# Optimization experiments

Measured on AMD Instinct MI355X. Metric: run time of the kernel, lower is better.

Reference implementation:

```python
import jax, jax.numpy as jnp
import numpy as np

B, N, C = 8, 900, 256
HEADS, P = 8, 4
BEV_H, BEV_W = 200, 200
RADIUS = 0.2


def setup_inputs() -> dict:
    key = jax.random.key(0)
    ks = jax.random.split(key, 6)
    return {
        'query': jax.random.normal(ks[0], (B, N, C), dtype=jnp.float32),
        'memory': jax.random.normal(ks[1], (B, BEV_H * BEV_W, C), dtype=jnp.float32),
        'reference_points': jax.random.uniform(ks[2], (B, N, 2), dtype=jnp.float32),
        'w_off': jax.random.normal(ks[3], (C, HEADS * P * 2), dtype=jnp.float32) * 0.02,
        'b_off': jnp.zeros((HEADS * P * 2,), jnp.float32),
        'w_wt': jax.random.normal(ks[4], (C, HEADS * P), dtype=jnp.float32) * 0.02,
        'b_wt': jnp.zeros((HEADS * P,), jnp.float32),
        'w_out': jax.random.normal(ks[5], (C, C), dtype=jnp.float32) * 0.02,
        'b_out': jnp.zeros((C,), jnp.float32),
        'bev_h': BEV_H,
        'bev_w': BEV_W,
    }


def reference(query, memory, reference_points, w_off, b_off, w_wt, b_wt, w_out, b_out, bev_h, bev_w):
    Bq, Nq, Cq = query.shape
    hd = Cq // HEADS
    # memory [B, H*W, C] -> per-head feature map flattened: [B, heads, HW, hd]
    feat = memory.transpose(0, 2, 1).reshape(Bq, HEADS, hd, bev_h * bev_w)
    feat = feat.transpose(0, 1, 3, 2)

    offsets = jnp.tanh(query @ w_off + b_off).reshape(Bq, Nq, HEADS, P, 2) * RADIUS
    weights = jax.nn.softmax((query @ w_wt + b_wt).reshape(Bq, Nq, HEADS, P), axis=-1)
    loc = reference_points[:, :, None, None, :2] + offsets  # [B,N,heads,P,2], normalized [0,1]

    # grid_sample(align_corners=False, zeros padding): pixel = p*size - 0.5
    x = loc[..., 0] * bev_w - 0.5
    y = loc[..., 1] * bev_h - 0.5
    x0f = jnp.floor(x)
    y0f = jnp.floor(y)
    x0 = x0f.astype(jnp.int32)
    y0 = y0f.astype(jnp.int32)
    fx = (x - x0f)[..., None]
    fy = (y - y0f)[..., None]

    def gather(xi, yi):
        valid = (xi >= 0) & (xi < bev_w) & (yi >= 0) & (yi < bev_h)
        idx = jnp.clip(yi, 0, bev_h - 1) * bev_w + jnp.clip(xi, 0, bev_w - 1)  # [B,N,heads,P]
        idx_t = idx.transpose(0, 2, 1, 3).reshape(Bq, HEADS, Nq * P)
        v = jnp.take_along_axis(feat, idx_t[..., None], axis=2)  # [B,heads,N*P,hd]
        v = v.reshape(Bq, HEADS, Nq, P, hd).transpose(0, 2, 1, 3, 4)  # [B,N,heads,P,hd]
        return v * valid.astype(v.dtype)[..., None]

    v00 = gather(x0, y0)
    v01 = gather(x0 + 1, y0)
    v10 = gather(x0, y0 + 1)
    v11 = gather(x0 + 1, y0 + 1)
    sampled = (v00 * (1 - fx) * (1 - fy) + v01 * fx * (1 - fy)
               + v10 * (1 - fx) * fy + v11 * fx * fy)  # [B,N,heads,P,hd]

    fused = (sampled * weights[..., None]).sum(axis=3).reshape(Bq, Nq, Cq)
    return fused @ w_out + b_out
```

## Files before the change

kernel.cpp:

```cpp
#include <hip/hip_runtime.h>
#include <math.h>

#define BB 8
#define NN 900
#define CC 256
#define HEADS 8
#define PP 4
#define BEV_H 200
#define BEV_W 200
#define HW (BEV_H * BEV_W)
#define HD 32
#define RADIUS 0.2f
#define M_TOT (BB * NN)

#define PROJ_AR 32
#define PROJ_BLOCKS (M_TOT / PROJ_AR)
#define PACK_BLOCKS 32
#define SR 16
#define SFS 280

typedef short s16x8 __attribute__((ext_vector_type(8)));
typedef float f32x4 __attribute__((ext_vector_type(4)));

static __device__ __forceinline__ unsigned short f2bf(float f) {
    unsigned int x = __float_as_uint(f);
    unsigned int r = x + 0x7FFFu + ((x >> 16) & 1u);
    return (unsigned short)(r >> 16);
}

__global__ __launch_bounds__(256) void proj_pack_kernel(
    const float* __restrict__ query,
    const float* __restrict__ refpts,
    const float* __restrict__ w_off,
    const float* __restrict__ b_off,
    const float* __restrict__ w_wt,
    const float* __restrict__ b_wt,
    const float* __restrict__ w_out,
    float* __restrict__ rec_w,
    int*   __restrict__ rec_i,
    unsigned short* __restrict__ Bp)
{
    const int t = threadIdx.x;

    if (blockIdx.x >= PROJ_BLOCKS) {
        const int g = (blockIdx.x - PROJ_BLOCKS) * 256 + t;
        const int n = g & 255, kg = g >> 8;
        unsigned int w[4];
        #pragma unroll
        for (int jj = 0; jj < 4; ++jj) {
            const unsigned int lo = f2bf(w_out[(size_t)(kg * 8 + jj * 2 + 0) * CC + n]);
            const unsigned int hi = f2bf(w_out[(size_t)(kg * 8 + jj * 2 + 1) * CC + n]);
            w[jj] = lo | (hi << 16);
        }
        uint4 v; v.x = w[0]; v.y = w[1]; v.z = w[2]; v.w = w[3];
        *(uint4*)&Bp[(size_t)g * 8] = v;
        return;
    }

    __shared__ float s_q[PROJ_AR][68];
    __shared__ float s_w[64][96];
    __shared__ float s_l[PROJ_AR][100];

    const int row0 = blockIdx.x * PROJ_AR;
    const int r  = t >> 3;
    const int cq = t & 7;

    float acc[12] = {};

    for (int k0 = 0; k0 < CC; k0 += 64) {
        __syncthreads();
        #pragma unroll
        for (int j = 0; j < 2; ++j) {
            const int e = (t + j * 256) * 4;
            const int rr = e >> 6, kk = e & 63;
            *(float4*)&s_q[rr][kk] =
                *(const float4*)&query[(size_t)(row0 + rr) * CC + k0 + kk];
        }
        #pragma unroll
        for (int j = 0; j < 4; ++j) {
            const int e = t + j * 256;
            const int kk = e >> 4, c4 = (e & 15) * 4;
            *(float4*)&s_w[kk][c4] =
                *(const float4*)&w_off[(size_t)(k0 + kk) * 64 + c4];
        }
        #pragma unroll
        for (int j = 0; j < 2; ++j) {
            const int e = t + j * 256;
            const int kk = e >> 3, c4 = (e & 7) * 4;
            *(float4*)&s_w[kk][64 + c4] =
                *(const float4*)&w_wt[(size_t)(k0 + kk) * 32 + c4];
        }
        __syncthreads();
        #pragma unroll 8
        for (int kk = 0; kk < 64; ++kk) {
            const float qv = s_q[r][kk];
            const float4 w0 = *(const float4*)&s_w[kk][cq * 12 + 0];
            const float4 w1 = *(const float4*)&s_w[kk][cq * 12 + 4];
            const float4 w2 = *(const float4*)&s_w[kk][cq * 12 + 8];
            acc[0]  += qv * w0.x; acc[1]  += qv * w0.y;
            acc[2]  += qv * w0.z; acc[3]  += qv * w0.w;
            acc[4]  += qv * w1.x; acc[5]  += qv * w1.y;
            acc[6]  += qv * w1.z; acc[7]  += qv * w1.w;
            acc[8]  += qv * w2.x; acc[9]  += qv * w2.y;
            acc[10] += qv * w2.z; acc[11] += qv * w2.w;
        }
    }

    #pragma unroll
    for (int j = 0; j < 12; ++j) {
        const int col = cq * 12 + j;
        const float bias = (col < 64) ? b_off[col] : b_wt[col - 64];
        s_l[r][col] = acc[j] + bias;
    }
    __syncthreads();

    {
        const int h = t & 7;
        const int bn = row0 + r;
        const float rx = refpts[(size_t)bn * 2 + 0];
        const float ry = refpts[(size_t)bn * 2 + 1];

        const float l0 = s_l[r][64 + h * 4 + 0];
        const float l1 = s_l[r][64 + h * 4 + 1];
        const float l2 = s_l[r][64 + h * 4 + 2];
        const float l3 = s_l[r][64 + h * 4 + 3];
        const float m = fmaxf(fmaxf(l0, l1), fmaxf(l2, l3));
        float e0 = expf(l0 - m), e1 = expf(l1 - m), e2 = expf(l2 - m), e3 = expf(l3 - m);
        const float inv = 1.f / (e0 + e1 + e2 + e3);
        float ww[4] = {e0 * inv, e1 * inv, e2 * inv, e3 * inv};

        #pragma unroll
        for (int p = 0; p < PP; ++p) {
            const float wt = ww[p];
            const float ox = tanhf(s_l[r][h * 8 + p * 2 + 0]) * RADIUS;
            const float oy = tanhf(s_l[r][h * 8 + p * 2 + 1]) * RADIUS;
            const float x = (rx + ox) * (float)BEV_W - 0.5f;
            const float y = (ry + oy) * (float)BEV_H - 0.5f;
            const float x0f = floorf(x), y0f = floorf(y);
            const int x0 = (int)x0f, y0 = (int)y0f;
            const float fx = x - x0f, fy = y - y0f;
            const bool xv0 = (unsigned)x0 < (unsigned)BEV_W;
            const bool xv1 = (unsigned)(x0 + 1) < (unsigned)BEV_W;
            const bool yv0 = (unsigned)y0 < (unsigned)BEV_H;
            const bool yv1 = (unsigned)(y0 + 1) < (unsigned)BEV_H;
            const int cx0 = min(max(x0, 0), BEV_W - 1);
            const int cx1 = min(max(x0 + 1, 0), BEV_W - 1);
            const int cy0 = min(max(y0, 0), BEV_H - 1);
            const int cy1 = min(max(y0 + 1, 0), BEV_H - 1);
            float4 wv;
            wv.x = (xv0 && yv0) ? wt * (1.f - fx) * (1.f - fy) : 0.f;
            wv.y = (xv1 && yv0) ? wt * fx * (1.f - fy) : 0.f;
            wv.z = (xv0 && yv1) ? wt * (1.f - fx) * fy : 0.f;
            wv.w = (xv1 && yv1) ? wt * fx * fy : 0.f;
            int4 iv;
            iv.x = cy0 * BEV_W + cx0; iv.y = cy0 * BEV_W + cx1;
            iv.z = cy1 * BEV_W + cx0; iv.w = cy1 * BEV_W + cx1;
            ((float4*)rec_w)[(size_t)bn * 32 + h * 4 + p] = wv;
            ((int4*)rec_i)[(size_t)bn * 32 + h * 4 + p] = iv;
        }
    }
}

__global__ __launch_bounds__(256, 2) void sample_gemm_kernel(
    const float* __restrict__ memory,
    const float* __restrict__ rec_w,
    const int*   __restrict__ rec_i,
    const unsigned short* __restrict__ Bp,
    const float* __restrict__ b_out,
    float* __restrict__ out)
{
    const int t = threadIdx.x;
    const int bn0 = blockIdx.x * SR;

    __shared__ float s_w[SR][128];
    __shared__ int   s_i[SR][128];
    __shared__ unsigned short s_f[SR * SFS];

    #pragma unroll
    for (int j = 0; j < 2; ++j) {
        const int e4 = (t + j * 256) * 4;
        const int q = e4 >> 7;
        const int h = (e4 >> 4) & 7;
        const int j0 = e4 & 15;
        const float4 wv = *(const float4*)&rec_w[(size_t)bn0 * 128 + e4];
        const int4   iv = *(const int4*)&rec_i[(size_t)bn0 * 128 + e4];
        s_w[q][(j0 + 0) * 8 + h] = wv.x; s_i[q][(j0 + 0) * 8 + h] = iv.x;
        s_w[q][(j0 + 1) * 8 + h] = wv.y; s_i[q][(j0 + 1) * 8 + h] = iv.y;
        s_w[q][(j0 + 2) * 8 + h] = wv.z; s_i[q][(j0 + 2) * 8 + h] = iv.z;
        s_w[q][(j0 + 3) * 8 + h] = wv.w; s_i[q][(j0 + 3) * 8 + h] = iv.w;
    }
    __syncthreads();

    {
        const int qg = t >> 6, h = (t >> 3) & 7, l8 = t & 7;
        const int coff = h * HD + l8 * 4;
        #pragma unroll
        for (int i = 0; i < 4; ++i) {
            const int ql = qg * 4 + i;
            const int bn = bn0 + ql;
            const int b = bn / NN;
            const float* mb = memory + (size_t)b * HW * CC + coff;
            float ax = 0.f, ay = 0.f, az = 0.f, aw = 0.f;
            #pragma unroll
            for (int j = 0; j < 16; ++j) {
                const float w = s_w[ql][j * 8 + h];
                const int idx = s_i[ql][j * 8 + h];
                const float4 v = *(const float4*)(mb + (size_t)idx * CC);
                ax += w * v.x; ay += w * v.y; az += w * v.z; aw += w * v.w;
            }
            ushort4 o; o.x = f2bf(ax); o.y = f2bf(ay); o.z = f2bf(az); o.w = f2bf(aw);
            *(ushort4*)&s_f[ql * SFS + coff] = o;
        }
    }
    __syncthreads();

    {
        const int lane = t & 63, wid = t >> 6;
        const int lr = lane & 15, lg = lane >> 4;
        const int n0w = wid * 64;
        f32x4 acc[4] = {};
        const unsigned short* Bb = Bp + ((size_t)lg * 256 + n0w + lr) * 8;
        const unsigned short* Ar = &s_f[lr * SFS + lg * 8];
        #pragma unroll
        for (int ks = 0; ks < 8; ++ks) {
            const s16x8 a = *(const s16x8*)(Ar + ks * 32);
            #pragma unroll
            for (int nt = 0; nt < 4; ++nt) {
                const s16x8 bv = *(const s16x8*)(Bb + (size_t)(ks * 4 * 256 + nt * 16) * 8);
                acc[nt] = __builtin_amdgcn_mfma_f32_16x16x32_bf16(a, bv, acc[nt], 0, 0, 0);
            }
        }
        #pragma unroll
        for (int nt = 0; nt < 4; ++nt) {
            const float bo = b_out[n0w + nt * 16 + lr];
            #pragma unroll
            for (int rr = 0; rr < 4; ++rr) {
                out[(size_t)(bn0 + lg * 4 + rr) * CC + n0w + nt * 16 + lr] = acc[nt][rr] + bo;
            }
        }
    }
}

extern "C" void kernel_launch(void* const* d_in, const int* in_sizes, int n_in,
                              void* d_out, int out_size, void* d_ws, size_t ws_size,
                              hipStream_t stream) {
    const float* query  = (const float*)d_in[0];
    const float* memory = (const float*)d_in[1];
    const float* refpts = (const float*)d_in[2];
    const float* w_off  = (const float*)d_in[3];
    const float* b_off  = (const float*)d_in[4];
    const float* w_wt   = (const float*)d_in[5];
    const float* b_wt   = (const float*)d_in[6];
    const float* w_out  = (const float*)d_in[7];
    const float* b_out  = (const float*)d_in[8];

    char* ws = (char*)d_ws;
    float*          rec_w = (float*)(ws);
    int*            rec_i = (int*)(ws + 3686400);
    unsigned short* Bp    = (unsigned short*)(ws + 7372800);
    float* out = (float*)d_out;

    proj_pack_kernel<<<PROJ_BLOCKS + PACK_BLOCKS, 256, 0, stream>>>(
        query, refpts, w_off, b_off, w_wt, b_wt, w_out, rec_w, rec_i, Bp);
    sample_gemm_kernel<<<M_TOT / SR, 256, 0, stream>>>(
        memory, rec_w, rec_i, Bp, b_out, out);
}
```

Baseline: 43.38 us.

## Fuse offset/weight projection into sampling kernel using split-bf16 MFMA

Moves the query projection (offsets and attention weights) from a separate FP32 SIMT kernel into the sampling+output GEMM kernel. It computes the projection per 16-row tile with bf16 MFMA, using hi/lo splitting (three products) to keep near-FP32 accuracy. Sampling records now stay in shared memory instead of making a round trip through global memory. The cost is more shared memory and work per block, plus a pack kernel that now also splits the projection weights.

New measurement: 35.66 us. -17.8%, faster.

```diff
diff --git a/kernel.cpp b/kernel.cpp
--- a/kernel.cpp
+++ b/kernel.cpp
@@ -13,10 +13,9 @@
 #define RADIUS 0.2f
 #define M_TOT (BB * NN)
 
-#define PROJ_AR 32
-#define PROJ_BLOCKS (M_TOT / PROJ_AR)
-#define PACK_BLOCKS 32
 #define SR 16
+#define QS 264
+#define RS 132
 #define SFS 280
 
 typedef short s16x8 __attribute__((ext_vector_type(8)));
@@ -27,23 +26,21 @@
     unsigned int r = x + 0x7FFFu + ((x >> 16) & 1u);
     return (unsigned short)(r >> 16);
 }
-
-__global__ __launch_bounds__(256) void proj_pack_kernel(
-    const float* __restrict__ query,
-    const float* __restrict__ refpts,
+static __device__ __forceinline__ float bf2f(unsigned short h) {
+    return __uint_as_float(((unsigned int)h) << 16);
+}
+
+__global__ __launch_bounds__(256) void pack_kernel(
     const float* __restrict__ w_off,
-    const float* __restrict__ b_off,
     const float* __restrict__ w_wt,
-    const float* __restrict__ b_wt,
     const float* __restrict__ w_out,
-    float* __restrict__ rec_w,
-    int*   __restrict__ rec_i,
+    unsigned short* __restrict__ Wp_hi,
+    unsigned short* __restrict__ Wp_lo,
     unsigned short* __restrict__ Bp)
 {
-    const int t = threadIdx.x;
-
-    if (blockIdx.x >= PROJ_BLOCKS) {
-        const int g = (blockIdx.x - PROJ_BLOCKS) * 256 + t;
+    const int t = threadIdx.x, blk = blockIdx.x;
+    if (blk < 32) {
+        const int g = blk * 256 + t;
         const int n = g & 255, kg = g >> 8;
         unsigned int w[4];
         #pragma unroll
@@ -54,86 +51,119 @@
         }
         uint4 v; v.x = w[0]; v.y = w[1]; v.z = w[2]; v.w = w[3];
         *(uint4*)&Bp[(size_t)g * 8] = v;
-        return;
-    }
-
-    __shared__ float s_q[PROJ_AR][68];
-    __shared__ float s_w[64][96];
-    __shared__ float s_l[PROJ_AR][100];
-
-    const int row0 = blockIdx.x * PROJ_AR;
-    const int r  = t >> 3;
-    const int cq = t & 7;
-
-    float acc[12] = {};
-
-    for (int k0 = 0; k0 < CC; k0 += 64) {
-        __syncthreads();
-        #pragma unroll
-        for (int j = 0; j < 2; ++j) {
-            const int e = (t + j * 256) * 4;
-            const int rr = e >> 6, kk = e & 63;
-            *(float4*)&s_q[rr][kk] =
-                *(const float4*)&query[(size_t)(row0 + rr) * CC + k0 + kk];
-        }
-        #pragma unroll
-        for (int j = 0; j < 4; ++j) {
-            const int e = t + j * 256;
-            const int kk = e >> 4, c4 = (e & 15) * 4;
-            *(float4*)&s_w[kk][c4] =
-                *(const float4*)&w_off[(size_t)(k0 + kk) * 64 + c4];
-        }
-        #pragma unroll
-        for (int j = 0; j < 2; ++j) {
-            const int e = t + j * 256;
-            const int kk = e >> 3, c4 = (e & 7) * 4;
-            *(float4*)&s_w[kk][64 + c4] =
-                *(const float4*)&w_wt[(size_t)(k0 + kk) * 32 + c4];
-        }
-        __syncthreads();
-        #pragma unroll 8
-        for (int kk = 0; kk < 64; ++kk) {
-            const float qv = s_q[r][kk];
-            const float4 w0 = *(const float4*)&s_w[kk][cq * 12 + 0];
-            const float4 w1 = *(const float4*)&s_w[kk][cq * 12 + 4];
-            const float4 w2 = *(const float4*)&s_w[kk][cq * 12 + 8];
-            acc[0]  += qv * w0.x; acc[1]  += qv * w0.y;
-            acc[2]  += qv * w0.z; acc[3]  += qv * w0.w;
-            acc[4]  += qv * w1.x; acc[5]  += qv * w1.y;
-            acc[6]  += qv * w1.z; acc[7]  += qv * w1.w;
-            acc[8]  += qv * w2.x; acc[9]  += qv * w2.y;
-            acc[10] += qv * w2.z; acc[11] += qv * w2.w;
-        }
-    }
+    } else {
+        const int gid = (blk - 32) * 256 + t;
+        const int kg = gid / 96, n = gid - kg * 96;
+        unsigned int wh[4], wl[4];
+        #pragma unroll
+        for (int jj = 0; jj < 4; ++jj) {
+            unsigned int hp[2], lp[2];
+            #pragma unroll
+            for (int s = 0; s < 2; ++s) {
+                const int k = kg * 8 + jj * 2 + s;
+                const float w = (n < 64) ? w_off[(size_t)k * 64 + n]
+                                         : w_wt[(size_t)k * 32 + (n - 64)];
+                const unsigned short h = f2bf(w);
+                hp[s] = h;
+                lp[s] = f2bf(w - bf2f(h));
+            }
+            wh[jj] = hp[0] | (hp[1] << 16);
+            wl[jj] = lp[0] | (lp[1] << 16);
+        }
+        uint4 vh; vh.x = wh[0]; vh.y = wh[1]; vh.z = wh[2]; vh.w = wh[3];
+        uint4 vl; vl.x = wl[0]; vl.y = wl[1]; vl.z = wl[2]; vl.w = wl[3];
+        *(uint4*)&Wp_hi[(size_t)gid * 8] = vh;
+        *(uint4*)&Wp_lo[(size_t)gid * 8] = vl;
+    }
+}
+
+__global__ __launch_bounds__(256, 2) void fused_kernel(
+    const float* __restrict__ query,
+    const float* __restrict__ refpts,
+    const float* __restrict__ memory,
+    const float* __restrict__ b_off,
+    const float* __restrict__ b_wt,
+    const float* __restrict__ b_out,
+    const unsigned short* __restrict__ Wp_hi,
+    const unsigned short* __restrict__ Wp_lo,
+    const unsigned short* __restrict__ Bp,
+    float* __restrict__ out)
+{
+    const int t = threadIdx.x;
+    const int bn0 = blockIdx.x * SR;
+    const int lane = t & 63, wid = t >> 6;
+    const int lr = lane & 15, lg = lane >> 4;
+
+    __shared__ unsigned short s_qhi[SR * QS];
+    __shared__ unsigned short s_qlo[SR * QS];
+    __shared__ float s_l[SR][100];
+    __shared__ float s_rw[SR * RS];
+    __shared__ int   s_ri[SR * RS];
+    __shared__ unsigned short s_f[SR * SFS];
 
     #pragma unroll
-    for (int j = 0; j < 12; ++j) {
-        const int col = cq * 12 + j;
-        const float bias = (col < 64) ? b_off[col] : b_wt[col - 64];
-        s_l[r][col] = acc[j] + bias;
-    }
-    __syncthreads();
-
-    {
-        const int h = t & 7;
-        const int bn = row0 + r;
+    for (int j = 0; j < 4; ++j) {
+        const int e4 = (t + j * 256) * 4;
+        const int r = e4 >> 8, c = e4 & 255;
+        const float4 q = *(const float4*)&query[(size_t)(bn0 + r) * CC + c];
+        ushort4 hv, lv;
+        hv.x = f2bf(q.x); lv.x = f2bf(q.x - bf2f(hv.x));
+        hv.y = f2bf(q.y); lv.y = f2bf(q.y - bf2f(hv.y));
+        hv.z = f2bf(q.z); lv.z = f2bf(q.z - bf2f(hv.z));
+        hv.w = f2bf(q.w); lv.w = f2bf(q.w - bf2f(hv.w));
+        *(ushort4*)&s_qhi[r * QS + c] = hv;
+        *(ushort4*)&s_qlo[r * QS + c] = lv;
+    }
+    __syncthreads();
+
+    if (wid < 3) {
+        f32x4 pa[2] = {};
+        #pragma unroll
+        for (int ks = 0; ks < 8; ++ks) {
+            const s16x8 ahi = *(const s16x8*)&s_qhi[lr * QS + lg * 8 + ks * 32];
+            const s16x8 alo = *(const s16x8*)&s_qlo[lr * QS + lg * 8 + ks * 32];
+            #pragma unroll
+            for (int n = 0; n < 2; ++n) {
+                const int nt = wid * 2 + n;
+                const size_t boff = ((size_t)(lg + ks * 4) * 96 + nt * 16 + lr) * 8;
+                const s16x8 bhi = *(const s16x8*)&Wp_hi[boff];
+                const s16x8 blo = *(const s16x8*)&Wp_lo[boff];
+                pa[n] = __builtin_amdgcn_mfma_f32_16x16x32_bf16(ahi, bhi, pa[n], 0, 0, 0);
+                pa[n] = __builtin_amdgcn_mfma_f32_16x16x32_bf16(ahi, blo, pa[n], 0, 0, 0);
+                pa[n] = __builtin_amdgcn_mfma_f32_16x16x32_bf16(alo, bhi, pa[n], 0, 0, 0);
+            }
+        }
+        #pragma unroll
+        for (int n = 0; n < 2; ++n) {
+            const int nt = wid * 2 + n;
+            #pragma unroll
+            for (int r = 0; r < 4; ++r)
+                s_l[lg * 4 + r][nt * 16 + lr] = pa[n][r];
+        }
+    }
+    __syncthreads();
+
+    if (t < SR * HEADS) {
+        const int r = t >> 3, h = t & 7;
+        const int bn = bn0 + r;
         const float rx = refpts[(size_t)bn * 2 + 0];
         const float ry = refpts[(size_t)bn * 2 + 1];
 
-        const float l0 = s_l[r][64 + h * 4 + 0];
-        const float l1 = s_l[r][64 + h * 4 + 1];
-        const float l2 = s_l[r][64 + h * 4 + 2];
-        const float l3 = s_l[r][64 + h * 4 + 3];
+        const float l0 = s_l[r][64 + h * 4 + 0] + b_wt[h * 4 + 0];
+        const float l1 = s_l[r][64 + h * 4 + 1] + b_wt[h * 4 + 1];
+        const float l2 = s_l[r][64 + h * 4 + 2] + b_wt[h * 4 + 2];
+        const float l3 = s_l[r][64 + h * 4 + 3] + b_wt[h * 4 + 3];
         const float m = fmaxf(fmaxf(l0, l1), fmaxf(l2, l3));
-        float e0 = expf(l0 - m), e1 = expf(l1 - m), e2 = expf(l2 - m), e3 = expf(l3 - m);
+        const float e0 = expf(l0 - m), e1 = expf(l1 - m);
+        const float e2 = expf(l2 - m), e3 = expf(l3 - m);
         const float inv = 1.f / (e0 + e1 + e2 + e3);
-        float ww[4] = {e0 * inv, e1 * inv, e2 * inv, e3 * inv};
+        const float ww[4] = {e0 * inv, e1 * inv, e2 * inv, e3 * inv};
 
         #pragma unroll
         for (int p = 0; p < PP; ++p) {
             const float wt = ww[p];
-            const float ox = tanhf(s_l[r][h * 8 + p * 2 + 0]) * RADIUS;
-            const float oy = tanhf(s_l[r][h * 8 + p * 2 + 1]) * RADIUS;
+            const float ox = tanhf(s_l[r][h * 8 + p * 2 + 0] + b_off[h * 8 + p * 2 + 0]) * RADIUS;
+            const float oy = tanhf(s_l[r][h * 8 + p * 2 + 1] + b_off[h * 8 + p * 2 + 1]) * RADIUS;
             const float x = (rx + ox) * (float)BEV_W - 0.5f;
             const float y = (ry + oy) * (float)BEV_H - 0.5f;
             const float x0f = floorf(x), y0f = floorf(y);
@@ -147,47 +177,16 @@
             const int cx1 = min(max(x0 + 1, 0), BEV_W - 1);
             const int cy0 = min(max(y0, 0), BEV_H - 1);
             const int cy1 = min(max(y0 + 1, 0), BEV_H - 1);
-            float4 wv;
-            wv.x = (xv0 && yv0) ? wt * (1.f - fx) * (1.f - fy) : 0.f;
-            wv.y = (xv1 && yv0) ? wt * fx * (1.f - fy) : 0.f;
-            wv.z = (xv0 && yv1) ? wt * (1.f - fx) * fy : 0.f;
-            wv.w = (xv1 && yv1) ? wt * fx * fy : 0.f;
-            int4 iv;
-            iv.x = cy0 * BEV_W + cx0; iv.y = cy0 * BEV_W + cx1;
-            iv.z = cy1 * BEV_W + cx0; iv.w = cy1 * BEV_W + cx1;
-            ((float4*)rec_w)[(size_t)bn * 32 + h * 4 + p] = wv;
-            ((int4*)rec_i)[(size_t)bn * 32 + h * 4 + p] = iv;
-        }
-    }
-}
-
-__global__ __launch_bounds__(256, 2) void sample_gemm_kernel(
-    const float* __restrict__ memory,
-    const float* __restrict__ rec_w,
-    const int*   __restrict__ rec_i,
-    const unsigned short* __restrict__ Bp,
-    const float* __restrict__ b_out,
-    float* __restrict__ out)
-{
-    const int t = threadIdx.x;
-    const int bn0 = blockIdx.x * SR;
-
-    __shared__ float s_w[SR][128];
-    __shared__ int   s_i[SR][128];
-    __shared__ unsigned short s_f[SR * SFS];
-
-    #pragma unroll
-    for (int j = 0; j < 2; ++j) {
-        const int e4 = (t + j * 256) * 4;
-        const int q = e4 >> 7;
-        const int h = (e4 >> 4) & 7;
-        const int j0 = e4 & 15;
-        const float4 wv = *(const float4*)&rec_w[(size_t)bn0 * 128 + e4];
-        const int4   iv = *(const int4*)&rec_i[(size_t)bn0 * 128 + e4];
-        s_w[q][(j0 + 0) * 8 + h] = wv.x; s_i[q][(j0 + 0) * 8 + h] = iv.x;
-        s_w[q][(j0 + 1) * 8 + h] = wv.y; s_i[q][(j0 + 1) * 8 + h] = iv.y;
-        s_w[q][(j0 + 2) * 8 + h] = wv.z; s_i[q][(j0 + 2) * 8 + h] = iv.z;
-        s_w[q][(j0 + 3) * 8 + h] = wv.w; s_i[q][(j0 + 3) * 8 + h] = iv.w;
+            const int base = r * RS + p * 32 + h;
+            s_rw[base + 0]  = (xv0 && yv0) ? wt * (1.f - fx) * (1.f - fy) : 0.f;
+            s_rw[base + 8]  = (xv1 && yv0) ? wt * fx * (1.f - fy) : 0.f;
+            s_rw[base + 16] = (xv0 && yv1) ? wt * (1.f - fx) * fy : 0.f;
+            s_rw[base + 24] = (xv1 && yv1) ? wt * fx * fy : 0.f;
+            s_ri[base + 0]  = cy0 * BEV_W + cx0;
+            s_ri[base + 8]  = cy0 * BEV_W + cx1;
+            s_ri[base + 16] = cy1 * BEV_W + cx0;
+            s_ri[base + 24] = cy1 * BEV_W + cx1;
+        }
     }
     __syncthreads();
 
@@ -203,8 +202,8 @@
             float ax = 0.f, ay = 0.f, az = 0.f, aw = 0.f;
             #pragma unroll
             for (int j = 0; j < 16; ++j) {
-                const float w = s_w[ql][j * 8 + h];
-                const int idx = s_i[ql][j * 8 + h];
+                const float w = s_rw[ql * RS + j * 8 + h];
+                const int idx = s_ri[ql * RS + j * 8 + h];
                 const float4 v = *(const float4*)(mb + (size_t)idx * CC);
                 ax += w * v.x; ay += w * v.y; az += w * v.z; aw += w * v.w;
             }
@@ -215,8 +214,6 @@
     __syncthreads();
 
     {
-        const int lane = t & 63, wid = t >> 6;
-        const int lr = lane & 15, lg = lane >> 4;
         const int n0w = wid * 64;
         f32x4 acc[4] = {};
         const unsigned short* Bb = Bp + ((size_t)lg * 256 + n0w + lr) * 8;
@@ -226,7 +223,7 @@
             const s16x8 a = *(const s16x8*)(Ar + ks * 32);
             #pragma unroll
             for (int nt = 0; nt < 4; ++nt) {
-                const s16x8 bv = *(const s16x8*)(Bb + (size_t)(ks * 4 * 256 + nt * 16) * 8);
+                const s16x8 bv = *(const s16x8*)(Bb + (size_t)(ks * 1024 + nt * 16) * 8);
                 acc[nt] = __builtin_amdgcn_mfma_f32_16x16x32_bf16(a, bv, acc[nt], 0, 0, 0);
             }
         }
@@ -255,13 +252,12 @@
     const float* b_out  = (const float*)d_in[8];
 
     char* ws = (char*)d_ws;
-    float*          rec_w = (float*)(ws);
-    int*            rec_i = (int*)(ws + 3686400);
-    unsigned short* Bp    = (unsigned short*)(ws + 7372800);
+    unsigned short* Bp    = (unsigned short*)(ws);
+    unsigned short* Wp_hi = (unsigned short*)(ws + 131072);
+    unsigned short* Wp_lo = (unsigned short*)(ws + 180224);
     float* out = (float*)d_out;
 
-    proj_pack_kernel<<<PROJ_BLOCKS + PACK_BLOCKS, 256, 0, stream>>>(
-        query, refpts, w_off, b_off, w_wt, b_wt, w_out, rec_w, rec_i, Bp);
-    sample_gemm_kernel<<<M_TOT / SR, 256, 0, stream>>>(
-        memory, rec_w, rec_i, Bp, b_out, out);
-}
+    pack_kernel<<<44, 256, 0, stream>>>(w_off, w_wt, w_out, Wp_hi, Wp_lo, Bp);
+    fused_kernel<<<M_TOT / SR, 256, 0, stream>>>(
+        query, refpts, memory, b_off, b_wt, b_out, Wp_hi, Wp_lo, Bp, out);
+}
```
